# Performance work log

Hardware: AMD Instinct MI355X
Metric: run time of the kernel (lower is better)

Reference implementation:

```python
import jax, jax.numpy as jnp
import numpy as np

H, W = 256, 512
SCORE_THR = 0.2
NMS_THR = 0.15
TOPK = 4096


def _make_anchors():
    xs = (np.arange(W) + 0.5) * 0.4 - 0.2 * W
    ys = (np.arange(H) + 0.5) * 0.4 - 0.2 * H
    gx, gy = np.meshgrid(xs, ys)            # [H, W]
    anc = np.zeros((H, W, 2, 7), dtype=np.float32)
    anc[..., 0] = gx[..., None]
    anc[..., 1] = gy[..., None]
    anc[..., 2] = -1.0
    anc[..., 3] = 1.56  # h
    anc[..., 4] = 1.6   # w
    anc[..., 5] = 3.9   # l
    anc[..., 0, 6] = 0.0
    anc[..., 1, 6] = np.pi / 2
    return jnp.asarray(anc)


def _make_T(theta, tx, ty, tz):
    c, s = np.cos(theta), np.sin(theta)
    T = np.eye(4, dtype=np.float32)
    T[0, 0], T[0, 1], T[1, 0], T[1, 1] = c, -s, s, c
    T[0, 3], T[1, 3], T[2, 3] = tx, ty, tz
    return jnp.asarray(T)


def setup_inputs() -> dict:
    key = jax.random.key(0)
    k1, k2, k3, k4 = jax.random.split(key, 4)
    return {
        "anchors": _make_anchors(),
        "psm_v": jax.random.normal(k1, (1, 2, H, W), jnp.float32),
        "rm_v": jax.random.normal(k2, (1, 14, H, W), jnp.float32) * 0.1,
        "psm_i": jax.random.normal(k3, (1, 2, H, W), jnp.float32),
        "rm_i": jax.random.normal(k4, (1, 14, H, W), jnp.float32) * 0.1,
        "t_proj": _make_T(0.05, 2.0, -1.0, 0.1),
        "t_ego": _make_T(-0.1, 5.0, 3.0, 0.0),
    }


def delta_to_boxes3d(rm, anchors):
    # rm: [1, 14, H, W] -> [A, 7]; anchors: [H, W, 2, 7] xyzhwlr -> [A, 7]
    d = jnp.transpose(rm[0], (1, 2, 0)).reshape(-1, 7)
    a = anchors.reshape(-1, 7)
    ad = jnp.sqrt(a[:, 4] ** 2 + a[:, 5] ** 2)          # diag of w,l
    xy = d[:, :2] * ad[:, None] + a[:, :2]
    z = d[:, 2] * a[:, 3] + a[:, 2]
    dims = jnp.exp(d[:, 3:6]) * a[:, 3:6]               # h, w, l
    yaw = d[:, 6] + a[:, 6]
    return jnp.concatenate([xy, z[:, None], dims, yaw[:, None]], axis=1)


def boxes_to_corners_3d(b):
    # b: [N, 7] x,y,z,h,w,l,yaw (order 'hwl') -> [N, 8, 3]
    h, w, l, yaw = b[:, 3], b[:, 4], b[:, 5], b[:, 6]
    sx = jnp.array([1, 1, -1, -1, 1, 1, -1, -1], jnp.float32) * 0.5
    sy = jnp.array([1, -1, -1, 1, 1, -1, -1, 1], jnp.float32) * 0.5
    sz = jnp.array([-1, -1, -1, -1, 1, 1, 1, 1], jnp.float32) * 0.5
    x = l[:, None] * sx
    y = w[:, None] * sy
    z = h[:, None] * sz
    c, s = jnp.cos(yaw)[:, None], jnp.sin(yaw)[:, None]
    xr = x * c - y * s + b[:, 0:1]
    yr = x * s + y * c + b[:, 1:2]
    zr = z + b[:, 2:3]
    return jnp.stack([xr, yr, zr], axis=-1)


def project_box3d(corners, T):
    # corners: [N, 8, 3]; T: [4, 4]
    return jnp.einsum('ij,nkj->nki', T[:3, :3], corners) + T[:3, 3]


def corner_to_center(corners):
    # inverse of boxes_to_corners_3d, order 'hwl'
    xyz = corners.mean(axis=1)
    h = corners[:, 4:, 2].mean(axis=1) - corners[:, :4, 2].mean(axis=1)
    dl = corners[:, (0, 1, 4, 5), :2] - corners[:, (3, 2, 7, 6), :2]
    dw = corners[:, (0, 3, 4, 7), :2] - corners[:, (1, 2, 5, 6), :2]
    l = jnp.linalg.norm(dl, axis=-1).mean(axis=1)
    w = jnp.linalg.norm(dw, axis=-1).mean(axis=1)
    d = dl.sum(axis=1)
    yaw = jnp.arctan2(d[:, 1], d[:, 0])
    return jnp.concatenate(
        [xyz, h[:, None], w[:, None], l[:, None], yaw[:, None]], axis=1)


def standup_boxes(corners):
    # [N, 8, 3] -> [N, 4] x1,y1,x2,y2 over BEV
    mn = corners[..., :2].min(axis=1)
    mx = corners[..., :2].max(axis=1)
    return jnp.concatenate([mn, mx], axis=1)


def iou_matrix(b):
    area = (b[:, 2] - b[:, 0]) * (b[:, 3] - b[:, 1])
    lt = jnp.maximum(b[:, None, :2], b[None, :, :2])
    rb = jnp.minimum(b[:, None, 2:], b[None, :, 2:])
    wh = jnp.clip(rb - lt, 0.0)
    inter = wh[..., 0] * wh[..., 1]
    return inter / (area[:, None] + area[None, :] - inter + 1e-6)


def nms_keep(iou, valid, thresh):
    K = iou.shape[0]
    idx = jnp.arange(K)

    def body(i, keep):
        sup = (iou[i] > thresh) & (idx > i) & keep[i]
        return keep & ~sup

    return jax.lax.fori_loop(0, K, body, valid)


def _branch(psm, rm, anchors):
    scores = jax.nn.sigmoid(jnp.transpose(psm[0], (1, 2, 0))).reshape(-1)
    boxes = delta_to_boxes3d(rm, anchors)
    return boxes, scores


def reference(anchors, psm_v, rm_v, psm_i, rm_i, t_proj, t_ego):
    boxes_v, scores_v = _branch(psm_v, rm_v, anchors)
    boxes_i, scores_i = _branch(psm_i, rm_i, anchors)
    # project infra branch boxes into ego frame via corner transform
    corners_i = boxes_to_corners_3d(boxes_i)
    boxes_i = corner_to_center(project_box3d(corners_i, t_proj))
    boxes = jnp.concatenate([boxes_v, boxes_i], axis=0)       # [2A, 7]
    scores = jnp.concatenate([scores_v, scores_i], axis=0)    # [2A]
    # project all to ego space
    proj = project_box3d(boxes_to_corners_3d(boxes), t_ego)   # [2A, 8, 3]
    # static replacement of masked_select: mask + top-K
    masked = jnp.where(scores > SCORE_THR, scores, -1.0)
    top_s, top_i = jax.lax.top_k(masked, TOPK)
    corners_k = proj[top_i]                                    # [K, 8, 3]
    iou = iou_matrix(standup_boxes(corners_k))
    keep = nms_keep(iou, top_s > SCORE_THR, NMS_THR)
    final = top_s * keep.astype(top_s.dtype)
    # pack corners + surviving scores: [K, 25]
    return jnp.concatenate([corners_k.reshape(TOPK, 24), final[:, None]], axis=1)
```

## Files before the change

kernel.cpp:

```cpp
#include <hip/hip_runtime.h>
#include <stdint.h>

typedef unsigned int u32;
typedef unsigned long long u64;

#define HH 256
#define WW 512
#define HW (HH*WW)
#define N2 (2*HW)
#define NT (2*N2)
#define TOPK 4096
#define SCORE_THR 0.2f
#define NMS_THR 0.15f

#define OFF_KEYS   0ull
#define OFF_GHIST  ((size_t)NT*4)
#define OFF_GHIST2 (OFF_GHIST + 4096)
#define OFF_CNT    (OFF_GHIST2 + 4096)
#define OFF_VALIDM (OFF_CNT + 16)
#define OFF_CAND   (OFF_VALIDM + 512)
#define OFF_STAND  OFF_CAND
#define OFF_SELIDX (OFF_CAND + 65536)
#define OFF_SELSC  (OFF_SELIDX + (size_t)TOPK*4)
#define OFF_TDIAG  (OFF_SELSC + (size_t)TOPK*4)
#define ZERO_BYTES (4096 + 4096 + 16)
#define RANK_J 8

__device__ __forceinline__ u32 f2ord(float f) {
    u32 b = __float_as_uint(f);
    return (b & 0x80000000u) ? ~b : (b | 0x80000000u);
}

__global__ void __launch_bounds__(1024) k_keys(const float* __restrict__ psm_v,
                                               const float* __restrict__ psm_i,
                                               u32* __restrict__ keys,
                                               u32* __restrict__ ghist) {
    __shared__ u32 lh[1024];
    int t = threadIdx.x;
    lh[t] = 0;
    __syncthreads();
    int n = blockIdx.x * 1024 + t;
    int br = n >> 18;
    int m  = n & (N2 - 1);
    int a  = m & 1;
    int hw = m >> 1;
    const float* psm = br ? psm_i : psm_v;
    float x = psm[a * HW + hw];
    float s = 1.0f / (1.0f + __builtin_expf(-x));
    u32 key = 0u;
    if (s > SCORE_THR) key = f2ord(s);
    keys[n] = key;
    if (key) atomicAdd(&lh[key >> 22], 1u);
    __syncthreads();
    u32 c = lh[t];
    if (c) atomicAdd(&ghist[t], c);
}

__device__ __forceinline__ void pivot1024(const u32* __restrict__ arr, u32 target,
                                          u32* out_bin, u32* out_next, int l) {
    u32 h[16], loc[16];
#pragma unroll
    for (int j = 0; j < 16; ++j) h[j] = arr[l * 16 + j];
    loc[15] = h[15];
#pragma unroll
    for (int j = 14; j >= 0; --j) loc[j] = loc[j + 1] + h[j];
    u32 T = loc[0];
    u32 incl = T;
#pragma unroll
    for (int d = 1; d < 64; d <<= 1) {
        u32 v = __shfl_down(incl, d);
        if (l + d < 64) incl += v;
    }
    u32 E = incl - T;
#pragma unroll
    for (int j = 0; j < 16; ++j) {
        u32 S  = loc[j] + E;
        u32 Sn = (j < 15 ? loc[j + 1] : 0u) + E;
        if (S >= target && Sn < target) {
            *out_bin = (u32)(l * 16 + j);
            *out_next = Sn;
        }
    }
}

__global__ void __launch_bounds__(1024) k_hist2(const u32* __restrict__ ghist,
                                                const u32* __restrict__ keys,
                                                u32* __restrict__ ghist2) {
    __shared__ u32 lh[1024];
    __shared__ u32 b1_sh;
    int tid = threadIdx.x;
    lh[tid] = 0;
    if (tid < 64) {
        u32 bin = 0xFFFFFFFFu, nxt = 0;
        pivot1024(ghist, (u32)TOPK, &bin, &nxt, tid);
        if (bin != 0xFFFFFFFFu) b1_sh = bin;
    }
    __syncthreads();
    u32 b1 = b1_sh;
    int n = blockIdx.x * 1024 + tid;
    u32 key = keys[n];
    if ((key >> 22) == b1) atomicAdd(&lh[(key >> 12) & 1023u], 1u);
    __syncthreads();
    u32 c = lh[tid];
    if (c) atomicAdd(&ghist2[tid], c);
}

__global__ void __launch_bounds__(1024) k_collect(const u32* __restrict__ ghist,
                                                  const u32* __restrict__ ghist2,
                                                  const u32* __restrict__ keys,
                                                  u64* __restrict__ cand,
                                                  u32* __restrict__ cnt) {
    __shared__ u32 b1_sh, t2_sh, b2_sh;
    int tid = threadIdx.x;
    if (tid < 64) {
        u32 bin = 0xFFFFFFFFu, nxt = 0;
        pivot1024(ghist, (u32)TOPK, &bin, &nxt, tid);
        if (bin != 0xFFFFFFFFu) { b1_sh = bin; t2_sh = (u32)TOPK - nxt; }
    }
    __syncthreads();
    if (tid < 64) {
        u32 bin = 0xFFFFFFFFu, nxt = 0;
        pivot1024(ghist2, t2_sh, &bin, &nxt, tid);
        if (bin != 0xFFFFFFFFu) b2_sh = bin;
    }
    __syncthreads();
    u32 thr20 = (b1_sh << 10) | b2_sh;
    int n = blockIdx.x * 1024 + tid;
    u32 key = keys[n];
    if ((key >> 12) >= thr20) {
        u32 pos = atomicAdd(cnt, 1u);
        if (pos < 8192u)
            cand[pos] = ((u64)key << 32) | (u64)(u32)(~(u32)n);
    }
}

__global__ void __launch_bounds__(256) k_rank1(const u64* __restrict__ cand,
                                               const u32* __restrict__ cnt,
                                               u32* __restrict__ partial) {
    __shared__ u64 tile[1024];
    int tid = threadIdx.x;
    int i = blockIdx.x * 256 + tid;
    u32 base = blockIdx.y * 1024u;
    u32 c = *cnt;
    if (c > 8192u) c = 8192u;
    u64 my = (i < (int)c) ? cand[i] : 0ull;
#pragma unroll
    for (int k = 0; k < 4; ++k) {
        u32 idx = base + tid + k * 256;
        tile[tid + k * 256] = (idx < c) ? cand[idx] : 0ull;
    }
    __syncthreads();
    u32 lim = (c > base) ? ((c - base < 1024u) ? (c - base) : 1024u) : 0u;
    u32 r = 0;
#pragma unroll 4
    for (u32 k = 0; k < lim; ++k) r += (tile[k] > my) ? 1u : 0u;
    partial[blockIdx.y * 8192 + i] = r;
}

__global__ void __launch_bounds__(256) k_scatter(const u64* __restrict__ cand,
                                                 const u32* __restrict__ cnt,
                                                 const u32* __restrict__ partial,
                                                 u32* __restrict__ sel_idx) {
    int i = blockIdx.x * 256 + threadIdx.x;
    u32 c = *cnt;
    if (c > 8192u) c = 8192u;
    if (i >= (int)c) return;
    u32 rank = 0;
#pragma unroll
    for (int bj = 0; bj < RANK_J; ++bj) rank += partial[bj * 8192 + i];
    if (rank < (u32)TOPK) {
        u64 my = cand[i];
        sel_idx[rank] = ~((u32)(my & 0xFFFFFFFFull));
    }
}

__device__ __forceinline__ void box_corners(const float b[7], float cx[8], float cy[8], float cz[8]) {
    const float sx[8] = {0.5f,0.5f,-0.5f,-0.5f,0.5f,0.5f,-0.5f,-0.5f};
    const float sy[8] = {0.5f,-0.5f,-0.5f,0.5f,0.5f,-0.5f,-0.5f,0.5f};
    const float sz[8] = {-0.5f,-0.5f,-0.5f,-0.5f,0.5f,0.5f,0.5f,0.5f};
    float c = __builtin_cosf(b[6]), s = __builtin_sinf(b[6]);
#pragma unroll
    for (int k = 0; k < 8; k++) {
        float x = b[5] * sx[k], y = b[4] * sy[k], z = b[3] * sz[k];
        cx[k] = x * c - y * s + b[0];
        cy[k] = x * s + y * c + b[1];
        cz[k] = z + b[2];
    }
}

__device__ __forceinline__ void proj_T(const float* __restrict__ T, float cx[8], float cy[8], float cz[8]) {
#pragma unroll
    for (int k = 0; k < 8; k++) {
        float x = cx[k], y = cy[k], z = cz[k];
        cx[k] = T[0] * x + T[1] * y + T[2]  * z + T[3];
        cy[k] = T[4] * x + T[5] * y + T[6]  * z + T[7];
        cz[k] = T[8] * x + T[9] * y + T[10] * z + T[11];
    }
}

__device__ __forceinline__ void corner_to_center(const float cx[8], const float cy[8], const float cz[8], float b[7]) {
    float mx = 0.f, my = 0.f, mz = 0.f;
#pragma unroll
    for (int k = 0; k < 8; k++) { mx += cx[k]; my += cy[k]; mz += cz[k]; }
    mx *= 0.125f; my *= 0.125f; mz *= 0.125f;
    float htop = (cz[4] + cz[5] + cz[6] + cz[7]) * 0.25f;
    float hbot = (cz[0] + cz[1] + cz[2] + cz[3]) * 0.25f;
    const int lA[4] = {0,1,4,5}, lB[4] = {3,2,7,6};
    const int wA[4] = {0,3,4,7}, wB[4] = {1,2,5,6};
    float l = 0.f, w = 0.f, dx = 0.f, dy = 0.f;
#pragma unroll
    for (int i = 0; i < 4; i++) {
        float ax = cx[lA[i]] - cx[lB[i]];
        float ay = cy[lA[i]] - cy[lB[i]];
        l += __builtin_sqrtf(ax * ax + ay * ay);
        dx += ax; dy += ay;
    }
#pragma unroll
    for (int i = 0; i < 4; i++) {
        float ax = cx[wA[i]] - cx[wB[i]];
        float ay = cy[wA[i]] - cy[wB[i]];
        w += __builtin_sqrtf(ax * ax + ay * ay);
    }
    b[0] = mx; b[1] = my; b[2] = mz;
    b[3] = htop - hbot;
    b[4] = w * 0.25f;
    b[5] = l * 0.25f;
    b[6] = atan2f(dy, dx);
}

__global__ void __launch_bounds__(256) k_boxes(const float* __restrict__ anchors,
                                               const float* __restrict__ psm_v,
                                               const float* __restrict__ psm_i,
                                               const float* __restrict__ rm_v,
                                               const float* __restrict__ rm_i,
                                               const float* __restrict__ tproj,
                                               const float* __restrict__ tego,
                                               const u32* __restrict__ sel_idx,
                                               float* __restrict__ sel_sc,
                                               float* __restrict__ out,
                                               float4* __restrict__ stand,
                                               u64* __restrict__ validm) {
    int k = blockIdx.x * blockDim.x + threadIdx.x;
    if (k >= TOPK) return;
    int n = (int)(sel_idx[k] & (u32)(NT - 1));
    int br = n >> 18;
    int m  = n & (N2 - 1);
    int a  = m & 1;
    int hw = m >> 1;

    const float* psm = br ? psm_i : psm_v;
    float xs = psm[a * HW + hw];
    float s  = 1.0f / (1.0f + __builtin_expf(-xs));
    sel_sc[k] = (s > SCORE_THR) ? s : -1.0f;
    u64 vbits = __ballot(s > SCORE_THR);
    if ((threadIdx.x & 63) == 0) validm[k >> 6] = vbits;

    const float* rm = br ? rm_i : rm_v;
    float d[7];
#pragma unroll
    for (int j = 0; j < 7; j++) d[j] = rm[(a * 7 + j) * HW + hw];
    const float* anc = anchors + (size_t)m * 7;
    float a0 = anc[0], a1 = anc[1], a2 = anc[2], a3 = anc[3], a4 = anc[4], a5 = anc[5], a6 = anc[6];
    float ad = __builtin_sqrtf(a4 * a4 + a5 * a5);
    float b[7];
    b[0] = d[0] * ad + a0;
    b[1] = d[1] * ad + a1;
    b[2] = d[2] * a3 + a2;
    b[3] = __builtin_expf(d[3]) * a3;
    b[4] = __builtin_expf(d[4]) * a4;
    b[5] = __builtin_expf(d[5]) * a5;
    b[6] = d[6] + a6;

    if (br) {
        float cx[8], cy[8], cz[8];
        box_corners(b, cx, cy, cz);
        proj_T(tproj, cx, cy, cz);
        corner_to_center(cx, cy, cz, b);
    }

    float cx[8], cy[8], cz[8];
    box_corners(b, cx, cy, cz);
    proj_T(tego, cx, cy, cz);

    float mnx = cx[0], mny = cy[0], mxx = cx[0], mxy = cy[0];
#pragma unroll
    for (int c = 0; c < 8; c++) {
        out[(size_t)k * 25 + c * 3 + 0] = cx[c];
        out[(size_t)k * 25 + c * 3 + 1] = cy[c];
        out[(size_t)k * 25 + c * 3 + 2] = cz[c];
        mnx = fminf(mnx, cx[c]); mny = fminf(mny, cy[c]);
        mxx = fmaxf(mxx, cx[c]); mxy = fmaxf(mxy, cy[c]);
    }
    stand[k] = make_float4(mnx, mny, mxx, mxy);
}

__global__ void __launch_bounds__(256) k_mask(const float4* __restrict__ stand,
                                              u64* __restrict__ mask) {
    int i = blockIdx.x * 4 + (threadIdx.x >> 6);
    int t = threadIdx.x & 63;
    int w0 = i >> 6;
    float4 bi = stand[i];
    float areai = (bi.z - bi.x) * (bi.w - bi.y);
    u64 myword = 0ull;
    for (int w = w0; w < 64; ++w) {
        int j = w * 64 + t;
        float4 bj = stand[j];
        float areaj = (bj.z - bj.x) * (bj.w - bj.y);
        float ltx = fmaxf(bi.x, bj.x), lty = fmaxf(bi.y, bj.y);
        float rbx = fminf(bi.z, bj.z), rby = fminf(bi.w, bj.w);
        float iw = fmaxf(rbx - ltx, 0.0f), ih = fmaxf(rby - lty, 0.0f);
        float inter = iw * ih;
        float iou = inter / (areai + areaj - inter + 1e-6f);
        bool sup = (iou > NMS_THR) && (j > i);
        u64 bits = __ballot(sup);
        if (t == w) myword = bits;
    }
    mask[(size_t)i * 64 + t] = myword;
}

__global__ void __launch_bounds__(64) k_diag(const float4* __restrict__ stand,
                                             u64* __restrict__ tdiag) {
    __shared__ float4 sb[64];
    int B = blockIdx.x, l = threadIdx.x;
    float4 me = stand[B * 64 + l];
    sb[l] = me;
    __syncthreads();
    float aream = (me.z - me.x) * (me.w - me.y);
    u64 T = 0ull;
    for (int j = 0; j < 64; ++j) {
        float4 bj = sb[j];
        float areaj = (bj.z - bj.x) * (bj.w - bj.y);
        float ltx = fmaxf(bj.x, me.x), lty = fmaxf(bj.y, me.y);
        float rbx = fminf(bj.z, me.z), rby = fminf(bj.w, me.w);
        float iw = fmaxf(rbx - ltx, 0.0f), ih = fmaxf(rby - lty, 0.0f);
        float inter = iw * ih;
        float iou = inter / (areaj + aream - inter + 1e-6f);
        bool sup = (iou > NMS_THR) && (j < l);
        T |= sup ? (1ull << j) : 0ull;
    }
    tdiag[B * 64 + l] = T;
}

__device__ __forceinline__ u64 readlane64(u64 v, int lane) {
    u32 lo = (u32)__builtin_amdgcn_readlane((int)(u32)v, lane);
    u32 hi = (u32)__builtin_amdgcn_readlane((int)(u32)(v >> 32), lane);
    return ((u64)hi << 32) | (u64)lo;
}

__device__ __forceinline__ void nms_prefetch(const u64* __restrict__ mask,
                                             const u64* __restrict__ tdiag,
                                             int c, int sw, int l,
                                             u64 (&buf)[16], u64& Tl) {
    Tl = tdiag[(size_t)c * 64 + l];
    const u64* rp = mask + (size_t)c * 4096 + (size_t)(sw * 16) * 64 + l;
#pragma unroll
    for (int k = 0; k < 16; ++k) buf[k] = rp[(size_t)k * 64];
}

__device__ __forceinline__ void nms_process(int B, int l, int sw,
                                            const u64 (&buf)[16], u64 Tl,
                                            u64 vreg, volatile u64* sh,
                                            u64& remv, u64& keep) {
    u64 x = readlane64(remv, B);
    if (l == 0) sh[(B & 1) * 4 + sw] = x;
    __asm__ volatile("" ::: "memory");
    __builtin_amdgcn_s_waitcnt(0xC07F);
    __builtin_amdgcn_s_barrier();
    __asm__ volatile("" ::: "memory");
    const volatile u64* s = sh + (B & 1) * 4;
    u64 curw = s[0] | s[1] | s[2] | s[3];
    u64 vm = readlane64(vreg, B);
    u64 ve = vm & ~curw;
    u64 D = 0ull, P = ve;
    while (D != P) {
        u64 nD = ve & ~__ballot((Tl & P) != 0ull);
        u64 nP = ve & ~__ballot((Tl & nD) != 0ull);
        D = nD; P = nP;
    }
    u64 kb = D;
    keep = (l == B) ? kb : keep;
    u64 kbw = kb >> (sw * 16);
    u64 p = 0ull;
#pragma unroll
    for (int k = 0; k < 16; ++k)
        p |= buf[k] & (0ull - ((kbw >> k) & 1ull));
    remv |= p;
}

__global__ void __launch_bounds__(256, 1) k_nms(const u64* __restrict__ mask,
                                                const u64* __restrict__ tdiag,
                                                const u64* __restrict__ validm,
                                                const float* __restrict__ sc,
                                                float* __restrict__ out) {
    __shared__ u64 sh[8];
    int l  = threadIdx.x & 63;
    int sw = __builtin_amdgcn_readfirstlane((int)(threadIdx.x >> 6));
    u64 remv = 0ull;
    u64 keep = 0ull;
    u64 vreg = validm[l];

    u64 b0[16], b1[16], b2[16], b3[16];
    u64 T0, T1, T2, T3;
    nms_prefetch(mask, tdiag, 0, sw, l, b0, T0);
    nms_prefetch(mask, tdiag, 1, sw, l, b1, T1);
    __builtin_amdgcn_sched_barrier(0);

    for (int m = 0; m < 16; ++m) {
        int B = m * 4;
        nms_prefetch(mask, tdiag, B + 2, sw, l, b2, T2);
        nms_prefetch(mask, tdiag, B + 3, sw, l, b3, T3);
        __builtin_amdgcn_sched_barrier(0);
        nms_process(B,     l, sw, b0, T0, vreg, sh, remv, keep);
        nms_process(B + 1, l, sw, b1, T1, vreg, sh, remv, keep);
        if (m < 15) {
            nms_prefetch(mask, tdiag, B + 4, sw, l, b0, T0);
            nms_prefetch(mask, tdiag, B + 5, sw, l, b1, T1);
        }
        __builtin_amdgcn_sched_barrier(0);
        nms_process(B + 2, l, sw, b2, T2, vreg, sh, remv, keep);
        nms_process(B + 3, l, sw, b3, T3, vreg, sh, remv, keep);
    }

    for (int k = 0; k < 16; ++k) {
        int c = sw * 16 + k;
        u64 kc = readlane64(keep, c);
        float s = sc[c * 64 + l];
        out[(size_t)(c * 64 + l) * 25 + 24] = ((kc >> l) & 1ull) ? s : 0.0f;
    }
}

extern "C" void kernel_launch(void* const* d_in, const int* in_sizes, int n_in,
                              void* d_out, int out_size, void* d_ws, size_t ws_size,
                              hipStream_t stream) {
    const float* anchors = (const float*)d_in[0];
    const float* psm_v   = (const float*)d_in[1];
    const float* rm_v    = (const float*)d_in[2];
    const float* psm_i   = (const float*)d_in[3];
    const float* rm_i    = (const float*)d_in[4];
    const float* tproj   = (const float*)d_in[5];
    const float* tego    = (const float*)d_in[6];
    float* out = (float*)d_out;
    char* ws = (char*)d_ws;

    u32*    keys    = (u32*)(ws + OFF_KEYS);
    u64*    mask    = (u64*)(ws + OFF_KEYS);
    u32*    partial = (u32*)(ws + OFF_KEYS);
    u32*    ghist   = (u32*)(ws + OFF_GHIST);
    u32*    ghist2  = (u32*)(ws + OFF_GHIST2);
    u32*    cnt     = (u32*)(ws + OFF_CNT);
    u64*    validm  = (u64*)(ws + OFF_VALIDM);
    u64*    cand    = (u64*)(ws + OFF_CAND);
    float4* stand   = (float4*)(ws + OFF_STAND);
    u32*    sel_idx = (u32*)(ws + OFF_SELIDX);
    float*  sel_sc  = (float*)(ws + OFF_SELSC);
    u64*    tdiag   = (u64*)(ws + OFF_TDIAG);

    hipMemsetAsync(ws + OFF_GHIST, 0, ZERO_BYTES, stream);
    k_keys   <<<NT / 1024, 1024, 0, stream>>>(psm_v, psm_i, keys, ghist);
    k_hist2  <<<NT / 1024, 1024, 0, stream>>>(ghist, keys, ghist2);
    k_collect<<<NT / 1024, 1024, 0, stream>>>(ghist, ghist2, keys, cand, cnt);
    k_rank1  <<<dim3(32, RANK_J), 256, 0, stream>>>(cand, cnt, partial);
    k_scatter<<<32, 256, 0, stream>>>(cand, cnt, partial, sel_idx);
    k_boxes  <<<TOPK / 256, 256, 0, stream>>>(anchors, psm_v, psm_i, rm_v, rm_i,
                                              tproj, tego, sel_idx, sel_sc, out,
                                              stand, validm);
    k_mask   <<<TOPK / 4, 256, 0, stream>>>(stand, mask);
    k_diag   <<<64, 64, 0, stream>>>(stand, tdiag);
    k_nms    <<<1, 256, 0, stream>>>(mask, tdiag, validm, sel_sc, out);
}
```

Before: 255.6 us.

## Split NMS rows across eight waves with deeper prefetch and triangular load skip

The single-block NMS kernel now runs eight waves instead of four, so each wave holds eight mask rows per chunk instead of sixteen. The prefetch pipeline deepens from two to four chunks ahead, and lanes below the diagonal skip loading mask words they never need. The aim is shorter per-wave serial work and better hiding of memory latency in this latency-bound kernel. The cost is more participants in each barrier and more shared-memory words to OR per step.

```diff
diff --git a/kernel.cpp b/kernel.cpp
--- a/kernel.cpp
+++ b/kernel.cpp
@@ -25,6 +25,8 @@
 #define OFF_TDIAG  (OFF_SELSC + (size_t)TOPK*4)
 #define ZERO_BYTES (4096 + 4096 + 16)
 #define RANK_J 8
+#define NMS_WAVES 8
+#define ROWS_PW 8
 
 __device__ __forceinline__ u32 f2ord(float f) {
     u32 b = __float_as_uint(f);
@@ -350,25 +352,32 @@
 __device__ __forceinline__ void nms_prefetch(const u64* __restrict__ mask,
                                              const u64* __restrict__ tdiag,
                                              int c, int sw, int l,
-                                             u64 (&buf)[16], u64& Tl) {
+                                             u64 (&buf)[ROWS_PW], u64& Tl) {
     Tl = tdiag[(size_t)c * 64 + l];
-    const u64* rp = mask + (size_t)c * 4096 + (size_t)(sw * 16) * 64 + l;
-#pragma unroll
-    for (int k = 0; k < 16; ++k) buf[k] = rp[(size_t)k * 64];
+    if (l >= c) {
+        const u64* rp = mask + (size_t)c * 4096 + (size_t)(sw * ROWS_PW) * 64 + l;
+#pragma unroll
+        for (int k = 0; k < ROWS_PW; ++k) buf[k] = rp[(size_t)k * 64];
+    } else {
+#pragma unroll
+        for (int k = 0; k < ROWS_PW; ++k) buf[k] = 0ull;
+    }
 }
 
 __device__ __forceinline__ void nms_process(int B, int l, int sw,
-                                            const u64 (&buf)[16], u64 Tl,
+                                            const u64 (&buf)[ROWS_PW], u64 Tl,
                                             u64 vreg, volatile u64* sh,
                                             u64& remv, u64& keep) {
     u64 x = readlane64(remv, B);
-    if (l == 0) sh[(B & 1) * 4 + sw] = x;
+    if (l == 0) sh[(B & 1) * NMS_WAVES + sw] = x;
     __asm__ volatile("" ::: "memory");
     __builtin_amdgcn_s_waitcnt(0xC07F);
     __builtin_amdgcn_s_barrier();
     __asm__ volatile("" ::: "memory");
-    const volatile u64* s = sh + (B & 1) * 4;
-    u64 curw = s[0] | s[1] | s[2] | s[3];
+    const volatile u64* s = sh + (B & 1) * NMS_WAVES;
+    u64 curw = 0ull;
+#pragma unroll
+    for (int w = 0; w < NMS_WAVES; ++w) curw |= s[w];
     u64 vm = readlane64(vreg, B);
     u64 ve = vm & ~curw;
     u64 D = 0ull, P = ve;
@@ -379,50 +388,63 @@
     }
     u64 kb = D;
     keep = (l == B) ? kb : keep;
-    u64 kbw = kb >> (sw * 16);
+    u64 kbw = kb >> (sw * ROWS_PW);
     u64 p = 0ull;
 #pragma unroll
-    for (int k = 0; k < 16; ++k)
+    for (int k = 0; k < ROWS_PW; ++k)
         p |= buf[k] & (0ull - ((kbw >> k) & 1ull));
     remv |= p;
 }
 
-__global__ void __launch_bounds__(256, 1) k_nms(const u64* __restrict__ mask,
-                                                const u64* __restrict__ tdiag,
-                                                const u64* __restrict__ validm,
-                                                const float* __restrict__ sc,
-                                                float* __restrict__ out) {
-    __shared__ u64 sh[8];
+__global__ void __launch_bounds__(NMS_WAVES * 64, 1)
+k_nms(const u64* __restrict__ mask,
+      const u64* __restrict__ tdiag,
+      const u64* __restrict__ validm,
+      const float* __restrict__ sc,
+      float* __restrict__ out) {
+    __shared__ u64 sh[2 * NMS_WAVES];
     int l  = threadIdx.x & 63;
     int sw = __builtin_amdgcn_readfirstlane((int)(threadIdx.x >> 6));
     u64 remv = 0ull;
     u64 keep = 0ull;
     u64 vreg = validm[l];
 
-    u64 b0[16], b1[16], b2[16], b3[16];
-    u64 T0, T1, T2, T3;
-    nms_prefetch(mask, tdiag, 0, sw, l, b0, T0);
-    nms_prefetch(mask, tdiag, 1, sw, l, b1, T1);
+    u64 a0[ROWS_PW], a1[ROWS_PW], a2[ROWS_PW], a3[ROWS_PW];
+    u64 b0[ROWS_PW], b1[ROWS_PW], b2[ROWS_PW], b3[ROWS_PW];
+    u64 Ta0, Ta1, Ta2, Ta3, Tb0, Tb1, Tb2, Tb3;
+
+    nms_prefetch(mask, tdiag, 0, sw, l, a0, Ta0);
+    nms_prefetch(mask, tdiag, 1, sw, l, a1, Ta1);
+    nms_prefetch(mask, tdiag, 2, sw, l, a2, Ta2);
+    nms_prefetch(mask, tdiag, 3, sw, l, a3, Ta3);
     __builtin_amdgcn_sched_barrier(0);
 
-    for (int m = 0; m < 16; ++m) {
-        int B = m * 4;
-        nms_prefetch(mask, tdiag, B + 2, sw, l, b2, T2);
-        nms_prefetch(mask, tdiag, B + 3, sw, l, b3, T3);
+    for (int m = 0; m < 8; ++m) {
+        int B = m * 8;
+        nms_prefetch(mask, tdiag, B + 4, sw, l, b0, Tb0);
+        nms_prefetch(mask, tdiag, B + 5, sw, l, b1, Tb1);
+        nms_prefetch(mask, tdiag, B + 6, sw, l, b2, Tb2);
+        nms_prefetch(mask, tdiag, B + 7, sw, l, b3, Tb3);
         __builtin_amdgcn_sched_barrier(0);
-        nms_process(B,     l, sw, b0, T0, vreg, sh, remv, keep);
-        nms_process(B + 1, l, sw, b1, T1, vreg, sh, remv, keep);
-        if (m < 15) {
-            nms_prefetch(mask, tdiag, B + 4, sw, l, b0, T0);
-            nms_prefetch(mask, tdiag, B + 5, sw, l, b1, T1);
+        nms_process(B,     l, sw, a0, Ta0, vreg, sh, remv, keep);
+        nms_process(B + 1, l, sw, a1, Ta1, vreg, sh, remv, keep);
+        nms_process(B + 2, l, sw, a2, Ta2, vreg, sh, remv, keep);
+        nms_process(B + 3, l, sw, a3, Ta3, vreg, sh, remv, keep);
+        if (m < 7) {
+            nms_prefetch(mask, tdiag, B + 8,  sw, l, a0, Ta0);
+            nms_prefetch(mask, tdiag, B + 9,  sw, l, a1, Ta1);
+            nms_prefetch(mask, tdiag, B + 10, sw, l, a2, Ta2);
+            nms_prefetch(mask, tdiag, B + 11, sw, l, a3, Ta3);
         }
         __builtin_amdgcn_sched_barrier(0);
-        nms_process(B + 2, l, sw, b2, T2, vreg, sh, remv, keep);
-        nms_process(B + 3, l, sw, b3, T3, vreg, sh, remv, keep);
-    }
-
-    for (int k = 0; k < 16; ++k) {
-        int c = sw * 16 + k;
+        nms_process(B + 4, l, sw, b0, Tb0, vreg, sh, remv, keep);
+        nms_process(B + 5, l, sw, b1, Tb1, vreg, sh, remv, keep);
+        nms_process(B + 6, l, sw, b2, Tb2, vreg, sh, remv, keep);
+        nms_process(B + 7, l, sw, b3, Tb3, vreg, sh, remv, keep);
+    }
+
+    for (int k = 0; k < ROWS_PW; ++k) {
+        int c = sw * ROWS_PW + k;
         u64 kc = readlane64(keep, c);
         float s = sc[c * 64 + l];
         out[(size_t)(c * 64 + l) * 25 + 24] = ((kc >> l) & 1ull) ? s : 0.0f;
@@ -466,5 +488,5 @@
                                               stand, validm);
     k_mask   <<<TOPK / 4, 256, 0, stream>>>(stand, mask);
     k_diag   <<<64, 64, 0, stream>>>(stand, tdiag);
-    k_nms    <<<1, 256, 0, stream>>>(mask, tdiag, validm, sel_sc, out);
-}
+    k_nms    <<<1, NMS_WAVES * 64, 0, stream>>>(mask, tdiag, validm, sel_sc, out);
+}
```

Result: slower. 265.3 us (+3.8%).

## Stream NMS mask rows into an LDS ring via async global_load_lds

Applied to the files above, without the earlier changes.

The single-block NMS kernel previously prefetched mask rows into four register buffers of sixteen u64 each. It now uses global_load_lds to asynchronously copy each column-block's mask rows and diagonal word into a three-slot LDS ring, staged three blocks ahead, and reads them back from LDS in each iteration. It also skips loading mask words for lanes whose columns fall below the current block, reducing global traffic. This is meant to cut register pressure and memory latency on the serial critical path, at the cost of LDS reads and waitcnt tuning that could stall if the hardcoded vmcnt encoding is off.

```diff
diff --git a/kernel.cpp b/kernel.cpp
--- a/kernel.cpp
+++ b/kernel.cpp
@@ -25,6 +25,11 @@
 #define OFF_TDIAG  (OFF_SELSC + (size_t)TOPK*4)
 #define ZERO_BYTES (4096 + 4096 + 16)
 #define RANK_J 8
+
+#define NMSW 4
+#define RPW 16
+#define WREG_U64 1088
+#define SLOT_U64 (NMSW * WREG_U64)
 
 __device__ __forceinline__ u32 f2ord(float f) {
     u32 b = __float_as_uint(f);
@@ -347,82 +352,85 @@
     return ((u64)hi << 32) | (u64)lo;
 }
 
-__device__ __forceinline__ void nms_prefetch(const u64* __restrict__ mask,
-                                             const u64* __restrict__ tdiag,
-                                             int c, int sw, int l,
-                                             u64 (&buf)[16], u64& Tl) {
-    Tl = tdiag[(size_t)c * 64 + l];
-    const u64* rp = mask + (size_t)c * 4096 + (size_t)(sw * 16) * 64 + l;
-#pragma unroll
-    for (int k = 0; k < 16; ++k) buf[k] = rp[(size_t)k * 64];
-}
-
-__device__ __forceinline__ void nms_process(int B, int l, int sw,
-                                            const u64 (&buf)[16], u64 Tl,
-                                            u64 vreg, volatile u64* sh,
-                                            u64& remv, u64& keep) {
-    u64 x = readlane64(remv, B);
-    if (l == 0) sh[(B & 1) * 4 + sw] = x;
-    __asm__ volatile("" ::: "memory");
-    __builtin_amdgcn_s_waitcnt(0xC07F);
-    __builtin_amdgcn_s_barrier();
-    __asm__ volatile("" ::: "memory");
-    const volatile u64* s = sh + (B & 1) * 4;
-    u64 curw = s[0] | s[1] | s[2] | s[3];
-    u64 vm = readlane64(vreg, B);
-    u64 ve = vm & ~curw;
-    u64 D = 0ull, P = ve;
-    while (D != P) {
-        u64 nD = ve & ~__ballot((Tl & P) != 0ull);
-        u64 nP = ve & ~__ballot((Tl & nD) != 0ull);
-        D = nD; P = nP;
-    }
-    u64 kb = D;
-    keep = (l == B) ? kb : keep;
-    u64 kbw = kb >> (sw * 16);
-    u64 p = 0ull;
-#pragma unroll
-    for (int k = 0; k < 16; ++k)
-        p |= buf[k] & (0ull - ((kbw >> k) & 1ull));
-    remv |= p;
-}
-
-__global__ void __launch_bounds__(256, 1) k_nms(const u64* __restrict__ mask,
-                                                const u64* __restrict__ tdiag,
-                                                const u64* __restrict__ validm,
-                                                const float* __restrict__ sc,
-                                                float* __restrict__ out) {
-    __shared__ u64 sh[8];
+__device__ __forceinline__ void nms_stage(const u64* __restrict__ mask,
+                                          const u64* __restrict__ tdiag,
+                                          int c, int s, int sw, int l,
+                                          u64* ring) {
+    u64* wb = ring + (size_t)s * SLOT_U64 + (size_t)sw * WREG_U64;
+    bool act = (2 * (l & 31) + 1) >= c;
+    const u64* gb = mask + (size_t)c * 4096 + (size_t)(sw * RPW) * 64 + (size_t)l * 2;
+    if (act) {
+#pragma unroll
+        for (int k = 0; k < 8; ++k) {
+            __builtin_amdgcn_global_load_lds(
+                (const __attribute__((address_space(1))) void*)(gb + k * 128),
+                (__attribute__((address_space(3))) void*)(wb + k * 128), 16, 0, 0);
+        }
+    }
+    if (l < 32) {
+        __builtin_amdgcn_global_load_lds(
+            (const __attribute__((address_space(1))) void*)(tdiag + (size_t)c * 64 + (size_t)l * 2),
+            (__attribute__((address_space(3))) void*)(wb + 1024), 16, 0, 0);
+    }
+}
+
+__global__ void __launch_bounds__(NMSW * 64, 1)
+k_nms(const u64* __restrict__ mask,
+      const u64* __restrict__ tdiag,
+      const u64* __restrict__ validm,
+      const float* __restrict__ sc,
+      float* __restrict__ out) {
+    __shared__ u64 ring[3 * SLOT_U64];
+    __shared__ u64 sh[2 * NMSW];
     int l  = threadIdx.x & 63;
     int sw = __builtin_amdgcn_readfirstlane((int)(threadIdx.x >> 6));
     u64 remv = 0ull;
     u64 keep = 0ull;
     u64 vreg = validm[l];
 
-    u64 b0[16], b1[16], b2[16], b3[16];
-    u64 T0, T1, T2, T3;
-    nms_prefetch(mask, tdiag, 0, sw, l, b0, T0);
-    nms_prefetch(mask, tdiag, 1, sw, l, b1, T1);
-    __builtin_amdgcn_sched_barrier(0);
-
-    for (int m = 0; m < 16; ++m) {
-        int B = m * 4;
-        nms_prefetch(mask, tdiag, B + 2, sw, l, b2, T2);
-        nms_prefetch(mask, tdiag, B + 3, sw, l, b3, T3);
+    nms_stage(mask, tdiag, 0, 0, sw, l, ring);
+    nms_stage(mask, tdiag, 1, 1, sw, l, ring);
+    nms_stage(mask, tdiag, 2, 2, sw, l, ring);
+
+    for (int B = 0; B < 64; ++B) {
+        int s = B % 3;
+        u64* wb = ring + (size_t)s * SLOT_U64 + (size_t)sw * WREG_U64;
+        u64 x = readlane64(remv, B);
+        if (l == 0) sh[(B & 1) * NMSW + sw] = x;
+        __asm__ volatile("" ::: "memory");
+        __builtin_amdgcn_s_waitcnt(0xC07F);
+        __builtin_amdgcn_s_barrier();
+        __asm__ volatile("" ::: "memory");
+        __builtin_amdgcn_s_waitcnt(0x4F72);
         __builtin_amdgcn_sched_barrier(0);
-        nms_process(B,     l, sw, b0, T0, vreg, sh, remv, keep);
-        nms_process(B + 1, l, sw, b1, T1, vreg, sh, remv, keep);
-        if (m < 15) {
-            nms_prefetch(mask, tdiag, B + 4, sw, l, b0, T0);
-            nms_prefetch(mask, tdiag, B + 5, sw, l, b1, T1);
+        __asm__ volatile("" ::: "memory");
+        const volatile u64* sp = sh + (B & 1) * NMSW;
+        u64 curw = sp[0] | sp[1] | sp[2] | sp[3];
+        u64 Tl = wb[1024 + l];
+        u64 row[RPW];
+#pragma unroll
+        for (int k = 0; k < RPW; ++k) row[k] = wb[(size_t)k * 64 + l];
+        u64 vm = readlane64(vreg, B);
+        u64 ve = vm & ~curw;
+        u64 D = 0ull, P = ve;
+        while (D != P) {
+            u64 nD = ve & ~__ballot((Tl & P) != 0ull);
+            u64 nP = ve & ~__ballot((Tl & nD) != 0ull);
+            D = nD; P = nP;
         }
-        __builtin_amdgcn_sched_barrier(0);
-        nms_process(B + 2, l, sw, b2, T2, vreg, sh, remv, keep);
-        nms_process(B + 3, l, sw, b3, T3, vreg, sh, remv, keep);
-    }
-
-    for (int k = 0; k < 16; ++k) {
-        int c = sw * 16 + k;
+        u64 kb = D;
+        keep = (l == B) ? kb : keep;
+        u64 kbw = (kb >> (sw * RPW)) & 0xFFFFull;
+        u64 p = 0ull;
+#pragma unroll
+        for (int k = 0; k < RPW; ++k)
+            p |= row[k] & (0ull - ((kbw >> k) & 1ull));
+        remv |= p;
+        if (B + 3 < 64) nms_stage(mask, tdiag, B + 3, s, sw, l, ring);
+    }
+
+    for (int k = 0; k < RPW; ++k) {
+        int c = sw * RPW + k;
         u64 kc = readlane64(keep, c);
         float s = sc[c * 64 + l];
         out[(size_t)(c * 64 + l) * 25 + 24] = ((kc >> l) & 1ull) ? s : 0.0f;
@@ -466,5 +474,5 @@
                                               stand, validm);
     k_mask   <<<TOPK / 4, 256, 0, stream>>>(stand, mask);
     k_diag   <<<64, 64, 0, stream>>>(stand, tdiag);
-    k_nms    <<<1, 256, 0, stream>>>(mask, tdiag, validm, sel_sc, out);
-}
+    k_nms    <<<1, NMSW * 64, 0, stream>>>(mask, tdiag, validm, sel_sc, out);
+}
```

Measured after the change: 244.1 us. -4.5%, faster.
